# Kernel tuning notes

Hardware: AMD Instinct MI355X
Metric: run time of the kernel (lower is better)

The kernel has to match this reference:

```python
import jax, jax.numpy as jnp
import numpy as np

B, C, T = 8, 512, 2048
INTER = C // 2            # inter_channels default = in_channels // 2
L = 2                     # temporal_layer_num


def _pos_encoding(c, t):
    # standard sinusoidal PE, returned as (c, t) to match pos().permute(0,2,1)
    pos = jnp.arange(t, dtype=jnp.float32)[:, None]            # (t,1)
    i = jnp.arange(0, c, 2, dtype=jnp.float32)                 # (c/2,)
    div = jnp.exp(-(jnp.log(10000.0) / c) * i)                 # (c/2,)
    pe = jnp.zeros((t, c), dtype=jnp.float32)
    pe = pe.at[:, 0::2].set(jnp.sin(pos * div))
    pe = pe.at[:, 1::2].set(jnp.cos(pos * div))
    return pe.T                                                # (c,t)


def _conv1x1(w, b, x):
    # kernel_size=1 Conv1d == channel GEMM: w (o,c), x (b,c,t) -> (b,o,t)
    return jnp.einsum('oc,bct->bot', w, x) + b[:, None]


def _temporal_conv(x, w, d):
    # Conv2d(1, c, kernel=(3, c), dilation=(d,1), padding=(d,0), no bias)
    # x (b,c,t) -> input (b,1,t,c); kernel w (c,3,c) -> (c,1,3,c); out (b,c,t,1)
    x4 = x.transpose(0, 2, 1)[:, None, :, :]
    k = w[:, None, :, :]
    y = jax.lax.conv_general_dilated(
        x4, k, window_strides=(1, 1), padding=((d, d), (0, 0)),
        rhs_dilation=(d, 1), dimension_numbers=('NCHW', 'OIHW', 'NCHW'))
    return y[..., 0]                                           # (b,c,t)


def setup_inputs() -> dict:
    key = jax.random.key(0)
    ks = jax.random.split(key, 12)
    n = lambda k, shape, s=0.02: jax.random.normal(k, shape, jnp.float32) * s
    return {
        'x': jax.random.normal(ks[0], (B, C, T), jnp.float32),
        'w_tr': n(ks[1], (C, C)),
        'b_tr': jnp.zeros((C,), jnp.float32),
        'w_tc': n(ks[2], (L, C, 3, C), 0.001),   # init.normal_(std=0.001)
        'w_g': n(ks[3], (L + 1, INTER, C)),
        'b_g': jnp.zeros((L + 1, INTER), jnp.float32),
        'w_th': n(ks[4], (L + 1, INTER, C)),
        'b_th': jnp.zeros((L + 1, INTER), jnp.float32),
        'w_ph': n(ks[5], (L + 1, INTER, C)),
        'b_ph': jnp.zeros((L + 1, INTER), jnp.float32),
        'w_W': n(ks[6], (C, INTER * (L + 1))),
        'b_W': jnp.zeros((C,), jnp.float32),
        'gamma': 1.0 + n(ks[7], (C,)),
        'beta': n(ks[8], (C,)),
    }


def reference(x, w_tr, b_tr, w_tc, w_g, b_g, w_th, b_th, w_ph, b_ph,
              w_W, b_W, gamma, beta):
    b, c, t = x.shape
    x = x + _pos_encoding(c, t)[None]                 # add positional encoding
    x = jax.nn.relu(_conv1x1(w_tr, b_tr, x))          # tranpos_w + relu

    # temporal dilated-conv features, then raw x as last branch
    temps = [_temporal_conv(x, w_tc[i], i + 1) for i in range(w_tc.shape[0])]
    temps.append(x)

    ys = []
    for i, tx in enumerate(temps):
        gx = _conv1x1(w_g[i], b_g[i], tx)             # (b,inter,t)
        th = _conv1x1(w_th[i], b_th[i], tx)           # (b,inter,t)
        ph = _conv1x1(w_ph[i], b_ph[i], tx)           # (b,inter,t)
        f = jax.nn.softmax(jnp.einsum('bit,bis->bts', th, ph), axis=-1)
        ys.append(jnp.einsum('bts,bis->bit', f, gx))  # (b,inter,t)

    y = jnp.concatenate(ys, axis=1)                   # (b, 3*inter, t)
    wy = _conv1x1(w_W, b_W, y)                        # (b,c,t)
    # BatchNorm1d, training-mode batch stats over (batch, time)
    mean = wy.mean(axis=(0, 2), keepdims=True)
    var = wy.var(axis=(0, 2), keepdims=True)
    wy = (wy - mean) * jax.lax.rsqrt(var + 1e-5)
    wy = wy * gamma[None, :, None] + beta[None, :, None]
    return wy + x
```

## Files before the change

### kernel.cpp

```cpp
#include <hip/hip_runtime.h>

#define B_ 8
#define C_ 512
#define T_ 2048
#define I_ 256
#define TP_ (T_ + 4)

typedef _Float16 f16x8 __attribute__((ext_vector_type(8)));
typedef float f32x4 __attribute__((ext_vector_type(4)));
typedef unsigned short u16;
typedef unsigned short u16x4 __attribute__((ext_vector_type(4)));

__device__ __forceinline__ u16 f2h(float f) {
    _Float16 h = (_Float16)f;
    return *(u16*)&h;
}
__device__ __forceinline__ float h2f(u16 u) {
    _Float16 h = *(_Float16*)&u;
    return (float)h;
}

#define AS1 __attribute__((address_space(1)))
#define AS3 __attribute__((address_space(3)))
__device__ __forceinline__ void gload16(const u16* g, u16* l) {
    __builtin_amdgcn_global_load_lds((const AS1 void*)(const void*)g,
                                     (AS3 void*)(void*)l, 16, 0, 0);
}

template <int WMODE, bool BIAS, bool RELU, bool TCONV>
__global__ __launch_bounds__(256) void mfma_gemm(
    const u16* __restrict__ A, long aB, int aZdiv, int lda,
    const u16* __restrict__ Bm, long bB, int ldb,
    const float* __restrict__ bias, int biasStride,
    float* __restrict__ Cf, u16* __restrict__ Cn, long cB, int ldc,
    u16* __restrict__ Ct, long ctB, int ldct, int ctOff,
    int K, int dShift)
{
    __shared__ u16 sA[128 * 64];
    __shared__ u16 sB[128 * 64];
    const int z = blockIdx.z;
    const int zw = z / aZdiv;
    const int m0 = blockIdx.y * 128, n0 = blockIdx.x * 128;
    const int tid = threadIdx.x;
    const int lane = tid & 63, wv = tid >> 6;
    const int wm = wv >> 1, wn = wv & 1;
    const int l15 = lane & 15, l4 = lane >> 4;

    const u16* Ab = A + (long)zw * aB + (long)m0 * lda;
    const u16* Bb = Bm + (long)z * bB + (long)n0 * ldb;

    const int srow = wv * 32 + (lane >> 3);
    const int sk16 = (lane & 7) ^ (lane >> 3);

    f32x4 acc[4][4];
    #pragma unroll
    for (int i = 0; i < 4; ++i)
        #pragma unroll
        for (int j = 0; j < 4; ++j) acc[i][j] = (f32x4){0.f, 0.f, 0.f, 0.f};

    for (int k0 = 0; k0 < K; k0 += 64) {
        int bCol = k0;
        int rOff = 0;
        if (TCONV) {
            const int kh = k0 >> 9;
            rOff = (kh - 1) * dShift;
            bCol = k0 & 511;
        }
        #pragma unroll
        for (int ch = 0; ch < 4; ++ch) {
            gload16(Ab + (long)(srow + ch * 8) * lda + k0 + sk16 * 8,
                    &sA[wv * 2048 + ch * 512]);
            gload16(Bb + (long)(srow + ch * 8 + rOff) * ldb + bCol + sk16 * 8,
                    &sB[wv * 2048 + ch * 512]);
        }
        __syncthreads();
        #pragma unroll
        for (int kk = 0; kk < 2; ++kk) {
            f16x8 af[4], bfr[4];
            #pragma unroll
            for (int f = 0; f < 4; ++f) {
                const int ra = wm * 64 + f * 16 + l15;
                af[f] = *(const f16x8*)&sA[ra * 64 + ((((kk << 2) | l4) ^ (ra & 7)) << 3)];
                const int rb = wn * 64 + f * 16 + l15;
                bfr[f] = *(const f16x8*)&sB[rb * 64 + ((((kk << 2) | l4) ^ (rb & 7)) << 3)];
            }
            #pragma unroll
            for (int mi = 0; mi < 4; ++mi)
                #pragma unroll
                for (int ni = 0; ni < 4; ++ni)
                    acc[mi][ni] = __builtin_amdgcn_mfma_f32_16x16x32_f16(
                        af[mi], bfr[ni], acc[mi][ni], 0, 0, 0);
        }
        __syncthreads();
    }

    #pragma unroll
    for (int mi = 0; mi < 4; ++mi) {
        const int mb = m0 + wm * 64 + mi * 16 + l4 * 4;
        float bv[4] = {0.f, 0.f, 0.f, 0.f};
        if (BIAS) {
            const float* bp = bias + (long)zw * biasStride;
            #pragma unroll
            for (int r = 0; r < 4; ++r) bv[r] = bp[mb + r];
        }
        #pragma unroll
        for (int ni = 0; ni < 4; ++ni) {
            const int nb = n0 + wn * 64 + ni * 16 + l15;
            float v[4];
            #pragma unroll
            for (int r = 0; r < 4; ++r) {
                v[r] = acc[mi][ni][r] + bv[r];
                if (RELU) v[r] = fmaxf(v[r], 0.f);
            }
            if (WMODE & 1) {
                #pragma unroll
                for (int r = 0; r < 4; ++r)
                    Cf[(long)z * cB + (long)(mb + r) * ldc + nb] = v[r];
            }
            if (WMODE & 2) {
                #pragma unroll
                for (int r = 0; r < 4; ++r)
                    Cn[(long)z * cB + (long)(mb + r) * ldc + nb] = f2h(v[r]);
            }
            if (WMODE & 4) {
                u16x4 pk;
                #pragma unroll
                for (int r = 0; r < 4; ++r) pk[r] = f2h(v[r]);
                *(u16x4*)&Ct[(long)z * ctB + (long)nb * ldct + ctOff + mb] = pk;
            }
        }
    }
}

__global__ __launch_bounds__(512) void flash_attn(
    const u16* __restrict__ thA, const u16* __restrict__ phA,
    const u16* __restrict__ gxA, u16* __restrict__ YT)
{
    __shared__ u16 sK[64 * 256];
    __shared__ u16 sV[256 * 64];
    __shared__ u16 sP[8 * 16 * 64];

    const int flat = blockIdx.y * 16 + blockIdx.x;
    const int swz = (flat & 7) * 48 + (flat >> 3);
    const int qb = swz & 15, z = swz >> 4;
    const int br = z >> 3, b = z & 7;
    const int t0 = qb * 128;
    const int tid = threadIdx.x;
    const int lane = tid & 63, wv = tid >> 6;
    const int l15 = lane & 15, l4 = lane >> 4;

    const u16* Qz = thA + (long)z * (T_ * I_);
    const u16* Kz = phA + (long)z * (T_ * I_);
    const u16* Vz = gxA + (long)z * ((long)I_ * T_);

    f16x8 qf[8];
    {
        const u16* qrow = Qz + (long)(t0 + wv * 16 + l15) * I_ + l4 * 8;
        #pragma unroll
        for (int ks = 0; ks < 8; ++ks) qf[ks] = *(const f16x8*)(qrow + ks * 32);
    }

    f32x4 oacc[16];
    #pragma unroll
    for (int i = 0; i < 16; ++i) oacc[i] = (f32x4){0.f, 0.f, 0.f, 0.f};
    float mrun[4] = {-1e30f, -1e30f, -1e30f, -1e30f};
    float lrun[4] = {0.f, 0.f, 0.f, 0.f};

    const int krow = tid >> 5;
    const int kk16 = (tid & 31) ^ (krow & 7);
    const int vrow = tid >> 3;
    const int vk16 = (tid & 7) ^ (vrow & 7);

    for (int s0 = 0; s0 < T_; s0 += 64) {
        #pragma unroll
        for (int is = 0; is < 4; ++is) {
            gload16(Kz + (long)(s0 + is * 16 + krow) * I_ + kk16 * 8,
                    &sK[is * 4096 + tid * 8]);
            gload16(Vz + (long)(is * 64 + vrow) * T_ + s0 + vk16 * 8,
                    &sV[is * 4096 + tid * 8]);
        }
        __syncthreads();

        f32x4 sacc[4];
        #pragma unroll
        for (int nf = 0; nf < 4; ++nf) sacc[nf] = (f32x4){0.f, 0.f, 0.f, 0.f};
        #pragma unroll
        for (int nf = 0; nf < 4; ++nf) {
            const int srow = nf * 16 + l15;
            #pragma unroll
            for (int ks = 0; ks < 8; ++ks) {
                f16x8 kf = *(const f16x8*)&sK[srow * 256 + ((((ks << 2) | l4) ^ (srow & 7)) << 3)];
                sacc[nf] = __builtin_amdgcn_mfma_f32_16x16x32_f16(qf[ks], kf, sacc[nf], 0, 0, 0);
            }
        }

        float scale[4];
        #pragma unroll
        for (int r = 0; r < 4; ++r) {
            float v0 = fmaxf(fmaxf(sacc[0][r], sacc[1][r]),
                             fmaxf(sacc[2][r], sacc[3][r]));
            #pragma unroll
            for (int o = 8; o; o >>= 1) v0 = fmaxf(v0, __shfl_xor(v0, o, 64));
            const float mnew = fmaxf(mrun[r], v0);
            scale[r] = __expf(mrun[r] - mnew);
            mrun[r] = mnew;
        }
        float rsum[4] = {0.f, 0.f, 0.f, 0.f};
        #pragma unroll
        for (int nf = 0; nf < 4; ++nf) {
            #pragma unroll
            for (int r = 0; r < 4; ++r) {
                const float p = __expf(sacc[nf][r] - mrun[r]);
                rsum[r] += p;
                const int tl = l4 * 4 + r;
                const int sl = l15 + nf * 16;
                sP[wv * 1024 + tl * 64 + ((((sl >> 3) ^ (tl & 7)) << 3) | (sl & 7))] = f2h(p);
            }
        }
        #pragma unroll
        for (int r = 0; r < 4; ++r) {
            #pragma unroll
            for (int o = 8; o; o >>= 1) rsum[r] += __shfl_xor(rsum[r], o, 64);
            lrun[r] = lrun[r] * scale[r] + rsum[r];
        }
        #pragma unroll
        for (int nf = 0; nf < 16; ++nf)
            #pragma unroll
            for (int r = 0; r < 4; ++r) oacc[nf][r] *= scale[r];

        f16x8 pa[2];
        #pragma unroll
        for (int kk = 0; kk < 2; ++kk)
            pa[kk] = *(const f16x8*)&sP[wv * 1024 + l15 * 64 + ((((kk << 2) | l4) ^ (l15 & 7)) << 3)];
        #pragma unroll
        for (int nf = 0; nf < 16; ++nf) {
            const int dvr = nf * 16 + l15;
            #pragma unroll
            for (int kk = 0; kk < 2; ++kk) {
                f16x8 vf = *(const f16x8*)&sV[dvr * 64 + ((((kk << 2) | l4) ^ (dvr & 7)) << 3)];
                oacc[nf] = __builtin_amdgcn_mfma_f32_16x16x32_f16(pa[kk], vf, oacc[nf], 0, 0, 0);
            }
        }
        __syncthreads();
    }

    #pragma unroll
    for (int r = 0; r < 4; ++r) {
        const float inv = 1.f / lrun[r];
        const int t = t0 + wv * 16 + l4 * 4 + r;
        u16* dst = YT + ((long)b * T_ + t) * (3 * I_) + br * I_ + l15;
        #pragma unroll
        for (int nf = 0; nf < 16; ++nf)
            dst[nf * 16] = f2h(oacc[nf][r] * inv);
    }
}

__global__ __launch_bounds__(256) void to_f16(
    const float* __restrict__ s, u16* __restrict__ d, long n4)
{
    const long i = (long)blockIdx.x * 256 + threadIdx.x;
    if (i >= n4) return;
    const float4 v = ((const float4*)s)[i];
    u16x4 pk = {f2h(v.x), f2h(v.y), f2h(v.z), f2h(v.w)};
    ((u16x4*)d)[i] = pk;
}

__global__ __launch_bounds__(256) void peT_kernel(float* __restrict__ peT)
{
    const int idx = blockIdx.x * 256 + threadIdx.x;
    const int c = idx & (C_ - 1), t = idx >> 9;
    const float i2 = (float)(c & ~1);
    const float freq = expf(-(9.210340371976184f / (float)C_) * i2);
    const float ang = (float)t * freq;
    peT[idx] = (c & 1) ? cosf(ang) : sinf(ang);
}

__global__ __launch_bounds__(256) void xpose_add(
    const float* __restrict__ x, const float* __restrict__ peT,
    u16* __restrict__ xpeT)
{
    __shared__ float tile[64][65];
    const int b = blockIdx.z;
    const int t0 = blockIdx.x * 64, c0 = blockIdx.y * 64;
    const int rr = threadIdx.x >> 4, cc4 = (threadIdx.x & 15) << 2;
    #pragma unroll
    for (int p = 0; p < 4; ++p) {
        const int row = rr + p * 16;
        const float4 v = *(const float4*)&x[((long)b * C_ + c0 + row) * T_ + t0 + cc4];
        tile[row][cc4 + 0] = v.x; tile[row][cc4 + 1] = v.y;
        tile[row][cc4 + 2] = v.z; tile[row][cc4 + 3] = v.w;
    }
    __syncthreads();
    #pragma unroll
    for (int p = 0; p < 4; ++p) {
        const int tt = rr + p * 16;
        const int gt = t0 + tt;
        const float4 pv = *(const float4*)&peT[(long)gt * C_ + c0 + cc4];
        u16x4 pk = {f2h(tile[cc4 + 0][tt] + pv.x),
                    f2h(tile[cc4 + 1][tt] + pv.y),
                    f2h(tile[cc4 + 2][tt] + pv.z),
                    f2h(tile[cc4 + 3][tt] + pv.w)};
        *(u16x4*)&xpeT[((long)b * T_ + gt) * C_ + c0 + cc4] = pk;
    }
}

__global__ __launch_bounds__(256) void stats_kernel(
    const float* __restrict__ wy, float* __restrict__ mean,
    float* __restrict__ rstd)
{
    __shared__ float sm[8];
    const int o = blockIdx.x, tid = threadIdx.x;
    float s = 0.f, ss = 0.f;
    for (int idx = tid; idx < B_ * T_; idx += 256) {
        const int b = idx >> 11, t = idx & (T_ - 1);
        const float vv = wy[((long)b * C_ + o) * T_ + t];
        s += vv; ss += vv * vv;
    }
    #pragma unroll
    for (int off = 32; off; off >>= 1) {
        s += __shfl_xor(s, off, 64);
        ss += __shfl_xor(ss, off, 64);
    }
    if ((tid & 63) == 0) { sm[tid >> 6] = s; sm[4 + (tid >> 6)] = ss; }
    __syncthreads();
    if (tid == 0) {
        s = sm[0] + sm[1] + sm[2] + sm[3];
        ss = sm[4] + sm[5] + sm[6] + sm[7];
        const float mu = s / (float)(B_ * T_);
        const float var = ss / (float)(B_ * T_) - mu * mu;
        mean[o] = mu;
        rstd[o] = rsqrtf(var + 1e-5f);
    }
}

__global__ __launch_bounds__(256) void final_kernel(
    float* __restrict__ out, const u16* __restrict__ x1n,
    const float* __restrict__ mean, const float* __restrict__ rstd,
    const float* __restrict__ gamma, const float* __restrict__ beta)
{
    const long i4 = (long)blockIdx.x * 256 + threadIdx.x;
    const long i = i4 * 4;
    const int c = (int)((i / T_) & (C_ - 1));
    const float4 w = ((const float4*)out)[i4];
    const uint2 xv = ((const uint2*)x1n)[i4];
    const u16* xb = (const u16*)&xv;
    const float mu = mean[c];
    const float a = rstd[c] * gamma[c];
    const float bb = beta[c];
    float4 r;
    r.x = (w.x - mu) * a + bb + h2f(xb[0]);
    r.y = (w.y - mu) * a + bb + h2f(xb[1]);
    r.z = (w.z - mu) * a + bb + h2f(xb[2]);
    r.w = (w.w - mu) * a + bb + h2f(xb[3]);
    ((float4*)out)[i4] = r;
}

extern "C" void kernel_launch(void* const* d_in, const int* in_sizes, int n_in,
                              void* d_out, int out_size, void* d_ws, size_t ws_size,
                              hipStream_t stream)
{
    const float* x    = (const float*)d_in[0];
    const float* w_tr = (const float*)d_in[1];
    const float* b_tr = (const float*)d_in[2];
    const float* w_tc = (const float*)d_in[3];
    const float* w_g  = (const float*)d_in[4];
    const float* b_g  = (const float*)d_in[5];
    const float* w_th = (const float*)d_in[6];
    const float* b_th = (const float*)d_in[7];
    const float* w_ph = (const float*)d_in[8];
    const float* b_ph = (const float*)d_in[9];
    const float* w_W  = (const float*)d_in[10];
    const float* b_W  = (const float*)d_in[11];
    const float* gamma = (const float*)d_in[12];
    const float* beta  = (const float*)d_in[13];
    float* out = (float*)d_out;

    char* pp = (char*)d_ws;
    auto nextp = [&](long bytes) { char* r = pp; pp += (bytes + 255) & ~255L; return r; };
    const long TC  = (long)T_ * C_;
    const long CT  = (long)C_ * T_;
    const long TPC = (long)TP_ * C_;
    const long TI  = (long)T_ * I_;
    const long IT  = (long)I_ * T_;

    float* peT  = (float*)nextp(4L * T_ * C_);
    u16* xpeT   = (u16*)nextp(2L * B_ * TC);
    u16* x1n    = (u16*)nextp(2L * B_ * CT);
    u16* txAll  = (u16*)nextp(2L * 3 * B_ * TPC);
    u16* gxAll  = (u16*)nextp(2L * 3 * B_ * IT);
    u16* thAll  = (u16*)nextp(2L * 3 * B_ * TI);
    u16* phAll  = (u16*)nextp(2L * 3 * B_ * TI);
    u16* YT     = (u16*)nextp(2L * B_ * T_ * 3 * I_);
    u16* w_trb  = (u16*)nextp(2L * C_ * C_);
    u16* w_tcb  = (u16*)nextp(2L * 2 * C_ * 3 * C_);
    u16* w_gb   = (u16*)nextp(2L * 3 * I_ * C_);
    u16* w_thb  = (u16*)nextp(2L * 3 * I_ * C_);
    u16* w_phb  = (u16*)nextp(2L * 3 * I_ * C_);
    u16* w_Wb   = (u16*)nextp(2L * C_ * 3 * I_);
    float* meanb = (float*)nextp(4L * C_);
    float* rstdb = (float*)nextp(4L * C_);

    u16* slab0 = txAll;
    u16* slab1 = txAll + B_ * TPC;
    u16* slab2 = txAll + 2L * B_ * TPC;

    auto cvt = [&](const float* s, u16* d, long n) {
        to_f16<<<(int)((n / 4 + 255) / 256), 256, 0, stream>>>(s, d, n / 4);
    };
    cvt(w_tr, w_trb, (long)C_ * C_);
    cvt(w_tc, w_tcb, 2L * C_ * 3 * C_);
    cvt(w_g,  w_gb,  3L * I_ * C_);
    cvt(w_th, w_thb, 3L * I_ * C_);
    cvt(w_ph, w_phb, 3L * I_ * C_);
    cvt(w_W,  w_Wb,  (long)C_ * 3 * I_);

    peT_kernel<<<(T_ * C_) / 256, 256, 0, stream>>>(peT);
    xpose_add<<<dim3(T_ / 64, C_ / 64, B_), 256, 0, stream>>>(x, peT, xpeT);

    hipMemsetAsync(slab2, 0, 2L * B_ * TPC, stream);

    mfma_gemm<6, true, true, false><<<dim3(16, 4, 8), 256, 0, stream>>>(
        w_trb, 0, 1, C_, xpeT, TC, C_, b_tr, 0,
        nullptr, x1n, CT, T_, slab2 + 2 * C_, TPC, C_, 0, C_, 0);

    mfma_gemm<4, false, false, true><<<dim3(16, 4, 8), 256, 0, stream>>>(
        w_tcb, 0, 1, 3 * C_, slab2 + 2 * C_, TPC, C_, nullptr, 0,
        nullptr, nullptr, 0, 0, slab0 + 2 * C_, TPC, C_, 0, 3 * C_, 1);
    mfma_gemm<4, false, false, true><<<dim3(16, 4, 8), 256, 0, stream>>>(
        w_tcb + (long)C_ * 3 * C_, 0, 1, 3 * C_, slab2 + 2 * C_, TPC, C_, nullptr, 0,
        nullptr, nullptr, 0, 0, slab1 + 2 * C_, TPC, C_, 0, 3 * C_, 2);

    mfma_gemm<2, true, false, false><<<dim3(16, 2, 24), 256, 0, stream>>>(
        w_gb, (long)I_ * C_, 8, C_, txAll + 2 * C_, TPC, C_, b_g, I_,
        nullptr, gxAll, IT, T_, nullptr, 0, 0, 0, C_, 0);
    mfma_gemm<4, true, false, false><<<dim3(16, 2, 24), 256, 0, stream>>>(
        w_thb, (long)I_ * C_, 8, C_, txAll + 2 * C_, TPC, C_, b_th, I_,
        nullptr, nullptr, 0, 0, thAll, TI, I_, 0, C_, 0);
    mfma_gemm<4, true, false, false><<<dim3(16, 2, 24), 256, 0, stream>>>(
        w_phb, (long)I_ * C_, 8, C_, txAll + 2 * C_, TPC, C_, b_ph, I_,
        nullptr, nullptr, 0, 0, phAll, TI, I_, 0, C_, 0);

    flash_attn<<<dim3(16, 24), 512, 0, stream>>>(thAll, phAll, gxAll, YT);

    mfma_gemm<1, true, false, false><<<dim3(16, 4, 8), 256, 0, stream>>>(
        w_Wb, 0, 1, 3 * I_, YT, (long)T_ * 3 * I_, 3 * I_, b_W, 0,
        out, nullptr, CT, T_, nullptr, 0, 0, 0, 3 * I_, 0);

    stats_kernel<<<C_, 256, 0, stream>>>(out, meanb, rstdb);
    final_kernel<<<(int)(B_ * C_ * T_ / 4 / 256), 256, 0, stream>>>(
        out, x1n, meanb, rstdb, gamma, beta);
}
```

Before: 511.0 us.

## Split flash attention along key dimension with a separate combine kernel

Splits each attention query block's key/value range into two halves processed by separate workgroups, doubling the grid from 384 to 768 blocks. Each half writes unnormalized fp16 partial outputs plus running max and sum, and a new combine kernel merges them with log-sum-exp rescaling into the final layout. This is meant to improve occupancy across the GPU's compute units. In exchange it adds an extra kernel launch, extra global traffic for the partials, and an additional fp16 rounding of unnormalized accumulators.

```diff
diff --git a/kernel.cpp b/kernel.cpp
--- a/kernel.cpp
+++ b/kernel.cpp
@@ -134,17 +134,20 @@
 
 __global__ __launch_bounds__(512) void flash_attn(
     const u16* __restrict__ thA, const u16* __restrict__ phA,
-    const u16* __restrict__ gxA, u16* __restrict__ YT)
+    const u16* __restrict__ gxA, u16* __restrict__ oH,
+    float* __restrict__ mH, float* __restrict__ lH)
 {
     __shared__ u16 sK[64 * 256];
     __shared__ u16 sV[256 * 64];
     __shared__ u16 sP[8 * 16 * 64];
 
-    const int flat = blockIdx.y * 16 + blockIdx.x;
-    const int swz = (flat & 7) * 48 + (flat >> 3);
-    const int qb = swz & 15, z = swz >> 4;
-    const int br = z >> 3, b = z & 7;
+    const int flat = (blockIdx.z * 24 + blockIdx.y) * 16 + blockIdx.x;
+    const int swz = (flat & 7) * 96 + (flat >> 3);
+    const int u = swz % 384;
+    const int qb = u & 15, z = u >> 4;
+    const int half = swz / 384;
     const int t0 = qb * 128;
+    const int sBase = half * (T_ / 2);
     const int tid = threadIdx.x;
     const int lane = tid & 63, wv = tid >> 6;
     const int l15 = lane & 15, l4 = lane >> 4;
@@ -171,7 +174,7 @@
     const int vrow = tid >> 3;
     const int vk16 = (tid & 7) ^ (vrow & 7);
 
-    for (int s0 = 0; s0 < T_; s0 += 64) {
+    for (int s0 = sBase; s0 < sBase + T_ / 2; s0 += 64) {
         #pragma unroll
         for (int is = 0; is < 4; ++is) {
             gload16(Kz + (long)(s0 + is * 16 + krow) * I_ + kk16 * 8,
@@ -246,13 +249,43 @@
 
     #pragma unroll
     for (int r = 0; r < 4; ++r) {
-        const float inv = 1.f / lrun[r];
         const int t = t0 + wv * 16 + l4 * 4 + r;
-        u16* dst = YT + ((long)b * T_ + t) * (3 * I_) + br * I_ + l15;
+        const long row = ((long)half * 24 + z) * T_ + t;
+        u16* dst = oH + row * I_ + l15;
         #pragma unroll
         for (int nf = 0; nf < 16; ++nf)
-            dst[nf * 16] = f2h(oacc[nf][r] * inv);
-    }
+            dst[nf * 16] = f2h(oacc[nf][r]);
+        if (l15 == 0) { mH[row] = mrun[r]; lH[row] = lrun[r]; }
+    }
+}
+
+__global__ __launch_bounds__(256) void combine_kernel(
+    const u16* __restrict__ oH, const float* __restrict__ mH,
+    const float* __restrict__ lH, u16* __restrict__ YT)
+{
+    const long idx = (long)blockIdx.x * 256 + threadIdx.x;
+    const int z = (int)(idx / (T_ * (I_ / 8)));
+    const long rem = idx % (T_ * (I_ / 8));
+    const int t = (int)(rem / (I_ / 8));
+    const int dv0 = (int)(rem % (I_ / 8)) * 8;
+    const long row0 = (long)z * T_ + t;
+    const long row1 = ((long)24 + z) * T_ + t;
+    const float m0 = mH[row0], m1 = mH[row1];
+    const float l0 = lH[row0], l1 = lH[row1];
+    const float m = fmaxf(m0, m1);
+    const float a0 = __expf(m0 - m), a1 = __expf(m1 - m);
+    const float inv = 1.f / (l0 * a0 + l1 * a1);
+    const uint4 p0 = *(const uint4*)&oH[row0 * I_ + dv0];
+    const uint4 p1 = *(const uint4*)&oH[row1 * I_ + dv0];
+    const u16* b0 = (const u16*)&p0;
+    const u16* b1 = (const u16*)&p1;
+    uint4 ov;
+    u16* bo = (u16*)&ov;
+    #pragma unroll
+    for (int j = 0; j < 8; ++j)
+        bo[j] = f2h((h2f(b0[j]) * a0 + h2f(b1[j]) * a1) * inv);
+    const int br = z >> 3, b = z & 7;
+    *(uint4*)&YT[((long)b * T_ + t) * (3 * I_) + br * I_ + dv0] = ov;
 }
 
 __global__ __launch_bounds__(256) void to_f16(
@@ -391,6 +424,9 @@
     u16* thAll  = (u16*)nextp(2L * 3 * B_ * TI);
     u16* phAll  = (u16*)nextp(2L * 3 * B_ * TI);
     u16* YT     = (u16*)nextp(2L * B_ * T_ * 3 * I_);
+    u16* oH     = (u16*)nextp(2L * 2 * 24 * T_ * I_);
+    float* mH   = (float*)nextp(4L * 2 * 24 * T_);
+    float* lH   = (float*)nextp(4L * 2 * 24 * T_);
     u16* w_trb  = (u16*)nextp(2L * C_ * C_);
     u16* w_tcb  = (u16*)nextp(2L * 2 * C_ * 3 * C_);
     u16* w_gb   = (u16*)nextp(2L * 3 * I_ * C_);
@@ -440,7 +476,8 @@
         w_phb, (long)I_ * C_, 8, C_, txAll + 2 * C_, TPC, C_, b_ph, I_,
         nullptr, nullptr, 0, 0, phAll, TI, I_, 0, C_, 0);
 
-    flash_attn<<<dim3(16, 24), 512, 0, stream>>>(thAll, phAll, gxAll, YT);
+    flash_attn<<<dim3(16, 24, 2), 512, 0, stream>>>(thAll, phAll, gxAll, oH, mH, lH);
+    combine_kernel<<<(int)(24L * T_ * (I_ / 8) / 256), 256, 0, stream>>>(oH, mH, lH, YT);
 
     mfma_gemm<1, true, false, false><<<dim3(16, 4, 8), 256, 0, stream>>>(
         w_Wb, 0, 1, 3 * I_, YT, (long)T_ * 3 * I_, 3 * I_, b_W, 0,
```

Result: faster. 481.4 us (-5.8%).
